# Performance work log

Measured on AMD Instinct MI355X. Metric: run time of the kernel, lower is better.

The kernel has to match this reference:

```python
import jax, jax.numpy as jnp
import numpy as np

N_NODES = 50000
N_EDGES = 800000
F_NODE = 128
F_EDGE = 64
Z_DIM = 2 * F_NODE + F_EDGE  # 320
BN_EPS = 1e-5


def _params(key):
    ks = jax.random.split(key, 16)
    s = 1.0 / np.sqrt(Z_DIM)
    p = {}
    for li, k4 in zip((1, 2), (ks[:8], ks[8:])):
        p[f"Wf{li}"] = jax.random.uniform(k4[0], (Z_DIM, F_NODE), jnp.float32, -s, s)
        p[f"bf{li}"] = jax.random.uniform(k4[1], (F_NODE,), jnp.float32, -s, s)
        p[f"Ws{li}"] = jax.random.uniform(k4[2], (Z_DIM, F_NODE), jnp.float32, -s, s)
        p[f"bs{li}"] = jax.random.uniform(k4[3], (F_NODE,), jnp.float32, -s, s)
        p[f"gamma{li}"] = jnp.ones((F_NODE,), jnp.float32)
        p[f"beta{li}"] = jnp.zeros((F_NODE,), jnp.float32)
        p[f"rmean{li}"] = jax.random.normal(k4[4], (F_NODE,), jnp.float32) * 0.1
        p[f"rvar{li}"] = jax.random.uniform(k4[5], (F_NODE,), jnp.float32, 0.5, 1.5)
    return p


def setup_inputs() -> dict:
    key = jax.random.key(0)
    k1, k2, k3, kp = jax.random.split(key, 4)
    inp = {
        "x": jax.random.normal(k1, (N_NODES, F_NODE), jnp.float32),
        "edge_index": jax.random.randint(k2, (2, N_EDGES), 0, N_NODES, jnp.int64),
        "edge_attr": jax.random.normal(k3, (N_EDGES, F_EDGE), jnp.float32),
    }
    inp.update(_params(kp))
    return inp


def _cgconv(x, src, dst, edge_attr, Wf, bf, Ws, bs, gamma, beta, rmean, rvar):
    # z = [x_i, x_j, edge_attr] with i = target (dst), j = source (src)
    z = jnp.concatenate([x[dst], x[src], edge_attr], axis=-1)  # [E, 320]
    msg = jax.nn.sigmoid(z @ Wf + bf) * jax.nn.softplus(z @ Ws + bs)  # [E, F]
    n = x.shape[0]
    summed = jax.ops.segment_sum(msg, dst, num_segments=n)  # [N, F]
    cnt = jax.ops.segment_sum(jnp.ones((dst.shape[0],), x.dtype), dst, num_segments=n)
    out = summed / jnp.maximum(cnt, 1.0)[:, None]  # mean aggregation
    out = (out - rmean) * jax.lax.rsqrt(rvar + BN_EPS) * gamma + beta  # BN (eval)
    return out + x  # residual


def reference(x, edge_index, edge_attr,
              Wf1, bf1, Ws1, bs1, gamma1, beta1, rmean1, rvar1,
              Wf2, bf2, Ws2, bs2, gamma2, beta2, rmean2, rvar2):
    src, dst = edge_index[0], edge_index[1]
    x = _cgconv(x, src, dst, edge_attr, Wf1, bf1, Ws1, bs1, gamma1, beta1, rmean1, rvar1)
    # dropout_p = 0.0 -> identity
    x = _cgconv(x, src, dst, edge_attr, Wf2, bf2, Ws2, bs2, gamma2, beta2, rmean2, rvar2)
    return x
```

## Files before the change

### kernel.cpp

```cpp
#include <hip/hip_runtime.h>
#include <math.h>

#define FN 128
#define FE 64
#define EPS 1e-5f

typedef __attribute__((ext_vector_type(8))) short bf16x8;
typedef __attribute__((ext_vector_type(4))) float f32x4;

__device__ __forceinline__ float bf2f(unsigned int u_low16) {
    union { unsigned int i; float f; } v; v.i = u_low16 << 16; return v.f;
}
__device__ __forceinline__ float bf2f_hi(unsigned int u) {
    union { unsigned int i; float f; } v; v.i = u & 0xffff0000u; return v.f;
}
__device__ __forceinline__ unsigned short f2bf(float f) {
    union { float f; unsigned int i; } v; v.f = f;
    unsigned int r = v.i + 0x7FFFu + ((v.i >> 16) & 1u);
    return (unsigned short)(r >> 16);
}
__device__ __forceinline__ unsigned int pack2bf(float a, float b) {
    return (unsigned int)f2bf(a) | ((unsigned int)f2bf(b) << 16);
}
__device__ __forceinline__ unsigned int pack4fp8(float a, float b, float c, float d) {
    int u = __builtin_amdgcn_cvt_pk_fp8_f32(a, b, 0, false);
    u = __builtin_amdgcn_cvt_pk_fp8_f32(c, d, u, true);
    return (unsigned int)u;
}
__device__ __forceinline__ float actfn(float f, float s) {
    float sig = __builtin_amdgcn_rcpf(1.0f + __expf(-f));
    float sp = fmaxf(s, 0.0f) + __logf(1.0f + __expf(-fabsf(s)));
    return sig * sp;
}

__global__ void hist_kernel(const int* __restrict__ edst, int* __restrict__ hist, int ne) {
    int e = blockIdx.x * 256 + threadIdx.x;
    if (e < ne) atomicAdd(&hist[edst[e]], 1);
}

__global__ __launch_bounds__(1024) void scan_kernel(
    const int* __restrict__ hist, int* __restrict__ cursor, int nn)
{
    __shared__ int buf[1024];
    int t = threadIdx.x;
    int per = (nn + 1023) >> 10;
    int lo = t * per, hi = min(lo + per, nn);
    int s = 0;
    for (int i = lo; i < hi; i++) s += hist[i];
    buf[t] = s;
    __syncthreads();
    int incl = s;
    for (int off = 1; off < 1024; off <<= 1) {
        int tmp = (t >= off) ? buf[t - off] : 0;
        __syncthreads();
        incl += tmp;
        buf[t] = incl;
        __syncthreads();
    }
    int run = incl - s;
    for (int i = lo; i < hi; i++) { cursor[i] = run; run += hist[i]; }
}

__global__ void scatter_kernel(const int* __restrict__ edst, int* __restrict__ cursor,
                               int* __restrict__ perm, int ne)
{
    int e = blockIdx.x * 256 + threadIdx.x;
    if (e < ne) {
        int pos = atomicAdd(&cursor[edst[e]], 1);
        perm[pos] = e;
    }
}

__global__ __launch_bounds__(256) void convert_ea_kernel(
    const float* __restrict__ EA, const int* __restrict__ perm,
    unsigned char* __restrict__ ea8, int ne)
{
    int pos = blockIdx.x * 256 + threadIdx.x;
    if (pos >= ne) return;
    const float* src = EA + (size_t)perm[pos] * FE;
    uint4 outv[4];
    unsigned int* o = (unsigned int*)outv;
#pragma unroll
    for (int q = 0; q < 16; q++) {
        float4 v = *(const float4*)(src + q * 4);
        o[q] = pack4fp8(v.x, v.y, v.z, v.w);
    }
    uint4* dst = (uint4*)(ea8 + (size_t)pos * 64);
#pragma unroll
    for (int q = 0; q < 4; q++) dst[q] = outv[q];
}

__global__ __launch_bounds__(256, 4) void node_gemm(
    const float* __restrict__ X, const float* __restrict__ Wf,
    const float* __restrict__ Ws, unsigned short* __restrict__ A, int nnodes)
{
    __shared__ unsigned short Xs[128][128];
    __shared__ unsigned short Wt[64][128];
    const int t = threadIdx.x;
    const int m0 = blockIdx.x * 128;
    const int c0 = blockIdx.y * 64;
    const int part = c0 >> 7;
    const float* Bsrc = ((part < 2) ? Wf : Ws) + (part & 1) * 128 * 128 + (c0 & 127);

    {
        int row = t & 127;
        int kh = t >> 7;
        int m = m0 + row;
        const float* src = X + (size_t)(m < nnodes ? m : 0) * FN + kh * 64;
        int swz = (row & 7) << 3;
#pragma unroll
        for (int q = 0; q < 8; q++) {
            float4 v0 = *(const float4*)(src + q * 8);
            float4 v1 = *(const float4*)(src + q * 8 + 4);
            unsigned int u0 = pack2bf(v0.x, v0.y), u1 = pack2bf(v0.z, v0.w);
            unsigned int u2 = pack2bf(v1.x, v1.y), u3 = pack2bf(v1.z, v1.w);
            int kk = (kh * 64 + q * 8) ^ swz;
            *(uint4*)&Xs[row][kk] = make_uint4(u0, u1, u2, u3);
        }
    }
    {
        int n = t & 63;
        int kq = t >> 6;
        int swz = (n & 7) << 3;
#pragma unroll
        for (int q = 0; q < 16; q++) {
            int k = kq * 32 + q * 2;
            unsigned int u = pack2bf(Bsrc[(size_t)k * FN + n], Bsrc[(size_t)(k + 1) * FN + n]);
            *(unsigned int*)&Wt[n][k ^ swz] = u;
        }
    }
    __syncthreads();

    const int wv = t >> 6, lane = t & 63;
    const int mw = (wv & 1) * 64;
    const int nw = (wv >> 1) * 32;
    f32x4 acc[4][2];
#pragma unroll
    for (int mt = 0; mt < 4; mt++)
#pragma unroll
        for (int nt = 0; nt < 2; nt++) acc[mt][nt] = (f32x4){0.f, 0.f, 0.f, 0.f};

#pragma unroll
    for (int ks = 0; ks < 4; ks++) {
        int kb = ks * 32 + ((lane >> 4) << 3);
        bf16x8 a[4], b[2];
#pragma unroll
        for (int mt = 0; mt < 4; mt++) {
            int row = mw + mt * 16 + (lane & 15);
            a[mt] = *(const bf16x8*)&Xs[row][kb ^ ((row & 7) << 3)];
        }
#pragma unroll
        for (int nt = 0; nt < 2; nt++) {
            int n = nw + nt * 16 + (lane & 15);
            b[nt] = *(const bf16x8*)&Wt[n][kb ^ ((n & 7) << 3)];
        }
#pragma unroll
        for (int mt = 0; mt < 4; mt++)
#pragma unroll
            for (int nt = 0; nt < 2; nt++)
                acc[mt][nt] = __builtin_amdgcn_mfma_f32_16x16x32_bf16(
                    a[mt], b[nt], acc[mt][nt], 0, 0, 0);
    }

#pragma unroll
    for (int mt = 0; mt < 4; mt++) {
        int m = m0 + mw + mt * 16 + ((lane >> 4) << 2);
#pragma unroll
        for (int nt = 0; nt < 2; nt++) {
            int n = c0 + nw + nt * 16 + (lane & 15);
#pragma unroll
            for (int r = 0; r < 4; r++)
                if (m + r < nnodes)
                    A[(size_t)(m + r) * 512 + n] = f2bf(acc[mt][nt][r]);
        }
    }
}

__global__ __launch_bounds__(256, 4) void edge_kernel(
    const unsigned short* __restrict__ A, const float* __restrict__ EA,
    const unsigned char* __restrict__ ea8,
    const int* __restrict__ esrc, const int* __restrict__ edst,
    const int* __restrict__ perm,
    const float* __restrict__ Wf, const float* __restrict__ Ws,
    const float* __restrict__ bfv, const float* __restrict__ bsv,
    float* __restrict__ summed, int nedges)
{
    __shared__ unsigned char Wlds[2][128][64];
    __shared__ unsigned short Ebuf[4][64][36];

    const int t = threadIdx.x;
    const int w = t >> 6, lane = t & 63;
    const int ebase = blockIdx.x * 256 + w * 64;

    {
        int col = t & 127;
        int half = t >> 7;
        int swz = (col & 7) << 3;
#pragma unroll 2
        for (int mat = 0; mat < 2; mat++) {
            const float* Wsrc = (mat == 0 ? Wf : Ws) + 256 * FN + col;
#pragma unroll
            for (int q = 0; q < 8; q++) {
                int k = half * 32 + q * 4;
                unsigned int u = pack4fp8(Wsrc[(size_t)k * FN],
                                          Wsrc[(size_t)(k + 1) * FN],
                                          Wsrc[(size_t)(k + 2) * FN],
                                          Wsrc[(size_t)(k + 3) * FN]);
                *(unsigned int*)&Wlds[mat][col][k ^ swz] = u;
            }
        }
    }

    int e = ebase + lane;
    bool valid = (e < nedges);
    int eC = valid ? e : (nedges - 1);
    const int pe = perm[eC];
    const int mydst = edst[pe];
    const int mysrc = esrc[pe];

    unsigned long long flushAfter;
    {
        int prevd = __shfl(mydst, (lane + 63) & 63);
        unsigned long long chg = __ballot(lane > 0 && (mydst != prevd));
        flushAfter = (chg >> 1) | (1ull << 63) | (1ull << 31);
    }

    int vmask[4];
    const unsigned short* dB[4];
    const unsigned short* sB[4];
#pragma unroll
    for (int nt = 0; nt < 4; nt++) {
        int el = nt * 16 + (lane & 15);
        vmask[nt] = (ebase + el < nedges) ? 1 : 0;
        int dn = __shfl(mydst, el);
        int sn = __shfl(mysrc, el);
        dB[nt] = A + (size_t)dn * 512;
        sB[nt] = A + (size_t)sn * 512 + 128;
    }

    long Eb[4][2];
    if (ea8) {
        const int koff8 = (lane >> 4) << 3;
#pragma unroll
        for (int nt = 0; nt < 4; nt++) {
            int row = ebase + nt * 16 + (lane & 15);
            if (row >= nedges) row = nedges - 1;
            const unsigned char* p = ea8 + (size_t)row * 64 + koff8;
            Eb[nt][0] = *(const long*)(const void*)(p);
            Eb[nt][1] = *(const long*)(const void*)(p + 32);
        }
    } else {
        const int koff = (lane >> 4) << 3;
#pragma unroll
        for (int nt = 0; nt < 4; nt++) {
            int el = nt * 16 + (lane & 15);
            int pr = __shfl(pe, el);
            const float* p = EA + (size_t)pr * FE + koff;
#pragma unroll
            for (int kk = 0; kk < 2; kk++) {
                float4 v0 = *(const float4*)(p + kk * 32);
                float4 v1 = *(const float4*)(p + kk * 32 + 4);
                unsigned int lo = pack4fp8(v0.x, v0.y, v0.z, v0.w);
                unsigned int hi = pack4fp8(v1.x, v1.y, v1.z, v1.w);
                Eb[nt][kk] = (long)(((unsigned long long)hi << 32) | lo);
            }
        }
    }
    __syncthreads();

    const int colo = (lane >> 4) << 2;
    const int cc = lane & 31;
    const int h = lane >> 5;

#pragma unroll 1
    for (int cb = 0; cb < 4; cb++) {
        const int c0 = cb * 32;

        uint2 gdf[4][2], gsf[4][2], gds[4][2], gss[4][2];
#pragma unroll
        for (int nt = 0; nt < 4; nt++)
#pragma unroll
            for (int mt = 0; mt < 2; mt++) {
                int off = c0 + mt * 16 + colo;
                gdf[nt][mt] = *(const uint2*)(const void*)(dB[nt] + off);
                gsf[nt][mt] = *(const uint2*)(const void*)(sB[nt] + off);
                gds[nt][mt] = *(const uint2*)(const void*)(dB[nt] + 256 + off);
                gss[nt][mt] = *(const uint2*)(const void*)(sB[nt] + 256 + off);
            }

        float4 bF[2], bS[2];
#pragma unroll
        for (int mt = 0; mt < 2; mt++) {
            bF[mt] = *(const float4*)(bfv + c0 + mt * 16 + colo);
            bS[mt] = *(const float4*)(bsv + c0 + mt * 16 + colo);
        }

        f32x4 accF[2][4], accS[2][4];
#pragma unroll
        for (int mt = 0; mt < 2; mt++)
#pragma unroll
            for (int nt = 0; nt < 4; nt++) {
                accF[mt][nt] = (f32x4){bF[mt].x, bF[mt].y, bF[mt].z, bF[mt].w};
                accS[mt][nt] = (f32x4){bS[mt].x, bS[mt].y, bS[mt].z, bS[mt].w};
            }
#pragma unroll
        for (int kk = 0; kk < 2; kk++) {
            long aF[2], aS[2];
#pragma unroll
            for (int mt = 0; mt < 2; mt++) {
                int col = c0 + mt * 16 + (lane & 15);
                int kidx = ((kk << 5) + ((lane >> 4) << 3)) ^ ((col & 7) << 3);
                aF[mt] = *(const long*)(const void*)&Wlds[0][col][kidx];
                aS[mt] = *(const long*)(const void*)&Wlds[1][col][kidx];
            }
#pragma unroll
            for (int mt = 0; mt < 2; mt++)
#pragma unroll
                for (int nt = 0; nt < 4; nt++) {
                    accF[mt][nt] = __builtin_amdgcn_mfma_f32_16x16x32_fp8_fp8(
                        aF[mt], Eb[nt][kk], accF[mt][nt], 0, 0, 0);
                    accS[mt][nt] = __builtin_amdgcn_mfma_f32_16x16x32_fp8_fp8(
                        aS[mt], Eb[nt][kk], accS[mt][nt], 0, 0, 0);
                }
        }

#pragma unroll
        for (int nt = 0; nt < 4; nt++) {
            int edge = nt * 16 + (lane & 15);
#pragma unroll
            for (int mt = 0; mt < 2; mt++) {
                f32x4 F = accF[mt][nt], S = accS[mt][nt];
                uint2 a0 = gdf[nt][mt], a1 = gsf[nt][mt];
                uint2 b0 = gds[nt][mt], b1 = gss[nt][mt];
                F[0] += bf2f(a0.x & 0xffffu) + bf2f(a1.x & 0xffffu);
                F[1] += bf2f_hi(a0.x)        + bf2f_hi(a1.x);
                F[2] += bf2f(a0.y & 0xffffu) + bf2f(a1.y & 0xffffu);
                F[3] += bf2f_hi(a0.y)        + bf2f_hi(a1.y);
                S[0] += bf2f(b0.x & 0xffffu) + bf2f(b1.x & 0xffffu);
                S[1] += bf2f_hi(b0.x)        + bf2f_hi(b1.x);
                S[2] += bf2f(b0.y & 0xffffu) + bf2f(b1.y & 0xffffu);
                S[3] += bf2f_hi(b0.y)        + bf2f_hi(b1.y);
                float m0 = actfn(F[0], S[0]);
                float m1 = actfn(F[1], S[1]);
                float m2 = actfn(F[2], S[2]);
                float m3 = actfn(F[3], S[3]);
                if (!vmask[nt]) { m0 = m1 = m2 = m3 = 0.0f; }
                uint2 mw = make_uint2(pack2bf(m0, m1), pack2bf(m2, m3));
                *(uint2*)&Ebuf[w][edge][mt * 16 + colo] = mw;
            }
        }

        asm volatile("" ::: "memory");

        {
            int ebit0 = h << 5;
            float run = 0.f;
#pragma unroll 1
            for (int q = 0; q < 32; q++) {
                int e2 = ebit0 + q;
                run += bf2f((unsigned int)Ebuf[w][e2][cc]);
                int d = __shfl(mydst, e2);
                if ((flushAfter >> e2) & 1ull) {
                    atomicAdd(&summed[(size_t)d * FN + c0 + cc], run);
                    run = 0.f;
                }
            }
        }

        asm volatile("" ::: "memory");
    }
}

__global__ __launch_bounds__(256) void finalize_kernel(
    const float* __restrict__ summed, const int* __restrict__ hist,
    const float* xin,
    const float* __restrict__ gamma, const float* __restrict__ beta,
    const float* __restrict__ rmean, const float* __restrict__ rvar,
    float* out, int nnodes)
{
    int idx = blockIdx.x * 256 + threadIdx.x;
    if (idx >= nnodes * FN) return;
    int n = idx >> 7, c = idx & (FN - 1);
    float cnt = (float)hist[n];
    float mean = summed[idx] / fmaxf(cnt, 1.0f);
    float y = (mean - rmean[c]) * rsqrtf(rvar[c] + EPS) * gamma[c] + beta[c] + xin[idx];
    out[idx] = y;
}

extern "C" void kernel_launch(void* const* d_in, const int* in_sizes, int n_in,
                              void* d_out, int out_size, void* d_ws, size_t ws_size,
                              hipStream_t stream)
{
    const float* x    = (const float*)d_in[0];
    const int*   eidx = (const int*)d_in[1];
    const float* ea   = (const float*)d_in[2];
    const float* Wf1 = (const float*)d_in[3],  * bf1 = (const float*)d_in[4];
    const float* Ws1 = (const float*)d_in[5],  * bs1 = (const float*)d_in[6];
    const float* g1  = (const float*)d_in[7],  * be1 = (const float*)d_in[8];
    const float* rm1 = (const float*)d_in[9],  * rv1 = (const float*)d_in[10];
    const float* Wf2 = (const float*)d_in[11], * bf2 = (const float*)d_in[12];
    const float* Ws2 = (const float*)d_in[13], * bs2 = (const float*)d_in[14];
    const float* g2  = (const float*)d_in[15], * be2 = (const float*)d_in[16];
    const float* rm2 = (const float*)d_in[17], * rv2 = (const float*)d_in[18];
    float* out = (float*)d_out;

    const int NN = in_sizes[0] / FN;
    const int NE = in_sizes[2] / FE;
    const int* esrc = eidx;
    const int* edst = eidx + NE;

    char* wsp = (char*)d_ws;
    unsigned short* A = (unsigned short*)wsp;            wsp += (size_t)NN * 512 * 2;
    float* summed     = (float*)wsp;                     wsp += (size_t)NN * FN * 4;
    int* hist         = (int*)wsp;                       wsp += (size_t)NN * 4;
    int* perm         = (int*)wsp;                       wsp += (size_t)NE * 4;
    size_t used       = (size_t)(wsp - (char*)d_ws);
    size_t needEA8    = used + (size_t)NE * 64;
    unsigned char* ea8 = (ws_size >= needEA8) ? (unsigned char*)wsp : nullptr;
    int* cursor       = (int*)summed;

    const int egrid = (NE + 255) / 256;
    const int ngrid = (NN + 127) / 128;
    const int fgrid = (NN * FN + 255) / 256;

    (void)hipMemsetAsync(hist, 0, (size_t)NN * 4, stream);
    hist_kernel<<<egrid, 256, 0, stream>>>(edst, hist, NE);
    scan_kernel<<<1, 1024, 0, stream>>>(hist, cursor, NN);
    scatter_kernel<<<egrid, 256, 0, stream>>>(edst, cursor, perm, NE);
    if (ea8) convert_ea_kernel<<<egrid, 256, 0, stream>>>(ea, perm, ea8, NE);

    (void)hipMemsetAsync(summed, 0, (size_t)NN * FN * 4, stream);
    node_gemm<<<dim3(ngrid, 8), 256, 0, stream>>>(x, Wf1, Ws1, A, NN);
    edge_kernel<<<egrid, 256, 0, stream>>>(A, ea, ea8, esrc, edst, perm, Wf1, Ws1, bf1, bs1, summed, NE);
    finalize_kernel<<<fgrid, 256, 0, stream>>>(summed, hist, x, g1, be1, rm1, rv1, out, NN);

    (void)hipMemsetAsync(summed, 0, (size_t)NN * FN * 4, stream);
    node_gemm<<<dim3(ngrid, 8), 256, 0, stream>>>(out, Wf2, Ws2, A, NN);
    edge_kernel<<<egrid, 256, 0, stream>>>(A, ea, ea8, esrc, edst, perm, Wf2, Ws2, bf2, bs2, summed, NE);
    finalize_kernel<<<fgrid, 256, 0, stream>>>(summed, hist, out, g2, be2, rm2, rv2, out, NN);
}
```

Baseline: 768.2 us.

## Store source-node projections in fp8 and convert edge attrs via inverse permutation

```diff
diff --git a/kernel.cpp b/kernel.cpp
--- a/kernel.cpp
+++ b/kernel.cpp
@@ -26,6 +26,9 @@
     int u = __builtin_amdgcn_cvt_pk_fp8_f32(a, b, 0, false);
     u = __builtin_amdgcn_cvt_pk_fp8_f32(c, d, u, true);
     return (unsigned int)u;
+}
+__device__ __forceinline__ unsigned char f2fp8(float v) {
+    return (unsigned char)(__builtin_amdgcn_cvt_pk_fp8_f32(v, v, 0, false) & 0xff);
 }
 __device__ __forceinline__ float actfn(float f, float s) {
     float sig = __builtin_amdgcn_rcpf(1.0f + __expf(-f));
@@ -62,22 +65,23 @@
 }
 
 __global__ void scatter_kernel(const int* __restrict__ edst, int* __restrict__ cursor,
-                               int* __restrict__ perm, int ne)
+                               int* __restrict__ perm, int* __restrict__ invp, int ne)
 {
     int e = blockIdx.x * 256 + threadIdx.x;
     if (e < ne) {
         int pos = atomicAdd(&cursor[edst[e]], 1);
         perm[pos] = e;
+        invp[e] = pos;
     }
 }
 
 __global__ __launch_bounds__(256) void convert_ea_kernel(
-    const float* __restrict__ EA, const int* __restrict__ perm,
+    const float* __restrict__ EA, const int* __restrict__ invp,
     unsigned char* __restrict__ ea8, int ne)
 {
-    int pos = blockIdx.x * 256 + threadIdx.x;
-    if (pos >= ne) return;
-    const float* src = EA + (size_t)perm[pos] * FE;
+    int e = blockIdx.x * 256 + threadIdx.x;
+    if (e >= ne) return;
+    const float* src = EA + (size_t)e * FE;
     uint4 outv[4];
     unsigned int* o = (unsigned int*)outv;
 #pragma unroll
@@ -85,14 +89,15 @@
         float4 v = *(const float4*)(src + q * 4);
         o[q] = pack4fp8(v.x, v.y, v.z, v.w);
     }
-    uint4* dst = (uint4*)(ea8 + (size_t)pos * 64);
+    uint4* dst = (uint4*)(ea8 + (size_t)invp[e] * 64);
 #pragma unroll
     for (int q = 0; q < 4; q++) dst[q] = outv[q];
 }
 
 __global__ __launch_bounds__(256, 4) void node_gemm(
     const float* __restrict__ X, const float* __restrict__ Wf,
-    const float* __restrict__ Ws, unsigned short* __restrict__ A, int nnodes)
+    const float* __restrict__ Ws, unsigned short* __restrict__ Ad,
+    unsigned char* __restrict__ As8, int nnodes)
 {
     __shared__ unsigned short Xs[128][128];
     __shared__ unsigned short Wt[64][128];
@@ -162,23 +167,29 @@
                     a[mt], b[nt], acc[mt][nt], 0, 0, 0);
     }
 
+    const int colbase = ((part >> 1) << 7) + (c0 & 127) + nw;
 #pragma unroll
     for (int mt = 0; mt < 4; mt++) {
         int m = m0 + mw + mt * 16 + ((lane >> 4) << 2);
 #pragma unroll
         for (int nt = 0; nt < 2; nt++) {
-            int n = c0 + nw + nt * 16 + (lane & 15);
-#pragma unroll
-            for (int r = 0; r < 4; r++)
-                if (m + r < nnodes)
-                    A[(size_t)(m + r) * 512 + n] = f2bf(acc[mt][nt][r]);
+            int col = colbase + nt * 16 + (lane & 15);
+#pragma unroll
+            for (int r = 0; r < 4; r++) {
+                if (m + r < nnodes) {
+                    if (part & 1)
+                        As8[(size_t)(m + r) * 256 + col] = f2fp8(acc[mt][nt][r]);
+                    else
+                        Ad[(size_t)(m + r) * 256 + col] = f2bf(acc[mt][nt][r]);
+                }
+            }
         }
     }
 }
 
 __global__ __launch_bounds__(256, 4) void edge_kernel(
-    const unsigned short* __restrict__ A, const float* __restrict__ EA,
-    const unsigned char* __restrict__ ea8,
+    const unsigned short* __restrict__ Ad, const unsigned char* __restrict__ As8,
+    const float* __restrict__ EA, const unsigned char* __restrict__ ea8,
     const int* __restrict__ esrc, const int* __restrict__ edst,
     const int* __restrict__ perm,
     const float* __restrict__ Wf, const float* __restrict__ Ws,
@@ -227,19 +238,19 @@
 
     int vmask[4];
     const unsigned short* dB[4];
-    const unsigned short* sB[4];
+    const unsigned char* sB[4];
 #pragma unroll
     for (int nt = 0; nt < 4; nt++) {
         int el = nt * 16 + (lane & 15);
         vmask[nt] = (ebase + el < nedges) ? 1 : 0;
         int dn = __shfl(mydst, el);
         int sn = __shfl(mysrc, el);
-        dB[nt] = A + (size_t)dn * 512;
-        sB[nt] = A + (size_t)sn * 512 + 128;
+        dB[nt] = Ad + (size_t)dn * 256;
+        sB[nt] = As8 + (size_t)sn * 256;
     }
 
     long Eb[4][2];
-    if (ea8) {
+    {
         const int koff8 = (lane >> 4) << 3;
 #pragma unroll
         for (int nt = 0; nt < 4; nt++) {
@@ -249,22 +260,6 @@
             Eb[nt][0] = *(const long*)(const void*)(p);
             Eb[nt][1] = *(const long*)(const void*)(p + 32);
         }
-    } else {
-        const int koff = (lane >> 4) << 3;
-#pragma unroll
-        for (int nt = 0; nt < 4; nt++) {
-            int el = nt * 16 + (lane & 15);
-            int pr = __shfl(pe, el);
-            const float* p = EA + (size_t)pr * FE + koff;
-#pragma unroll
-            for (int kk = 0; kk < 2; kk++) {
-                float4 v0 = *(const float4*)(p + kk * 32);
-                float4 v1 = *(const float4*)(p + kk * 32 + 4);
-                unsigned int lo = pack4fp8(v0.x, v0.y, v0.z, v0.w);
-                unsigned int hi = pack4fp8(v1.x, v1.y, v1.z, v1.w);
-                Eb[nt][kk] = (long)(((unsigned long long)hi << 32) | lo);
-            }
-        }
     }
     __syncthreads();
 
@@ -276,16 +271,17 @@
     for (int cb = 0; cb < 4; cb++) {
         const int c0 = cb * 32;
 
-        uint2 gdf[4][2], gsf[4][2], gds[4][2], gss[4][2];
+        uint2 gdf[4][2], gds[4][2];
+        unsigned int gsf8[4][2], gss8[4][2];
 #pragma unroll
         for (int nt = 0; nt < 4; nt++)
 #pragma unroll
             for (int mt = 0; mt < 2; mt++) {
                 int off = c0 + mt * 16 + colo;
                 gdf[nt][mt] = *(const uint2*)(const void*)(dB[nt] + off);
-                gsf[nt][mt] = *(const uint2*)(const void*)(sB[nt] + off);
-                gds[nt][mt] = *(const uint2*)(const void*)(dB[nt] + 256 + off);
-                gss[nt][mt] = *(const uint2*)(const void*)(sB[nt] + 256 + off);
+                gds[nt][mt] = *(const uint2*)(const void*)(dB[nt] + 128 + off);
+                gsf8[nt][mt] = *(const unsigned int*)(const void*)(sB[nt] + off);
+                gss8[nt][mt] = *(const unsigned int*)(const void*)(sB[nt] + 128 + off);
             }
 
         float4 bF[2], bS[2];
@@ -330,16 +326,16 @@
 #pragma unroll
             for (int mt = 0; mt < 2; mt++) {
                 f32x4 F = accF[mt][nt], S = accS[mt][nt];
-                uint2 a0 = gdf[nt][mt], a1 = gsf[nt][mt];
-                uint2 b0 = gds[nt][mt], b1 = gss[nt][mt];
-                F[0] += bf2f(a0.x & 0xffffu) + bf2f(a1.x & 0xffffu);
-                F[1] += bf2f_hi(a0.x)        + bf2f_hi(a1.x);
-                F[2] += bf2f(a0.y & 0xffffu) + bf2f(a1.y & 0xffffu);
-                F[3] += bf2f_hi(a0.y)        + bf2f_hi(a1.y);
-                S[0] += bf2f(b0.x & 0xffffu) + bf2f(b1.x & 0xffffu);
-                S[1] += bf2f_hi(b0.x)        + bf2f_hi(b1.x);
-                S[2] += bf2f(b0.y & 0xffffu) + bf2f(b1.y & 0xffffu);
-                S[3] += bf2f_hi(b0.y)        + bf2f_hi(b1.y);
+                uint2 a0 = gdf[nt][mt], b0 = gds[nt][mt];
+                unsigned int a1 = gsf8[nt][mt], b1 = gss8[nt][mt];
+                F[0] += bf2f(a0.x & 0xffffu) + __builtin_amdgcn_cvt_f32_fp8(a1, 0);
+                F[1] += bf2f_hi(a0.x)        + __builtin_amdgcn_cvt_f32_fp8(a1, 1);
+                F[2] += bf2f(a0.y & 0xffffu) + __builtin_amdgcn_cvt_f32_fp8(a1, 2);
+                F[3] += bf2f_hi(a0.y)        + __builtin_amdgcn_cvt_f32_fp8(a1, 3);
+                S[0] += bf2f(b0.x & 0xffffu) + __builtin_amdgcn_cvt_f32_fp8(b1, 0);
+                S[1] += bf2f_hi(b0.x)        + __builtin_amdgcn_cvt_f32_fp8(b1, 1);
+                S[2] += bf2f(b0.y & 0xffffu) + __builtin_amdgcn_cvt_f32_fp8(b1, 2);
+                S[3] += bf2f_hi(b0.y)        + __builtin_amdgcn_cvt_f32_fp8(b1, 3);
                 float m0 = actfn(F[0], S[0]);
                 float m1 = actfn(F[1], S[1]);
                 float m2 = actfn(F[2], S[2]);
@@ -410,13 +406,13 @@
     const int* edst = eidx + NE;
 
     char* wsp = (char*)d_ws;
-    unsigned short* A = (unsigned short*)wsp;            wsp += (size_t)NN * 512 * 2;
+    unsigned short* Ad  = (unsigned short*)wsp;          wsp += (size_t)NN * 256 * 2;
+    unsigned char*  As8 = (unsigned char*)wsp;           wsp += (size_t)NN * 256;
     float* summed     = (float*)wsp;                     wsp += (size_t)NN * FN * 4;
     int* hist         = (int*)wsp;                       wsp += (size_t)NN * 4;
     int* perm         = (int*)wsp;                       wsp += (size_t)NE * 4;
-    size_t used       = (size_t)(wsp - (char*)d_ws);
-    size_t needEA8    = used + (size_t)NE * 64;
-    unsigned char* ea8 = (ws_size >= needEA8) ? (unsigned char*)wsp : nullptr;
+    int* invp         = (int*)wsp;                       wsp += (size_t)NE * 4;
+    unsigned char* ea8 = (unsigned char*)wsp;            wsp += (size_t)NE * 64;
     int* cursor       = (int*)summed;
 
     const int egrid = (NE + 255) / 256;
@@ -426,16 +422,16 @@
     (void)hipMemsetAsync(hist, 0, (size_t)NN * 4, stream);
     hist_kernel<<<egrid, 256, 0, stream>>>(edst, hist, NE);
     scan_kernel<<<1, 1024, 0, stream>>>(hist, cursor, NN);
-    scatter_kernel<<<egrid, 256, 0, stream>>>(edst, cursor, perm, NE);
-    if (ea8) convert_ea_kernel<<<egrid, 256, 0, stream>>>(ea, perm, ea8, NE);
+    scatter_kernel<<<egrid, 256, 0, stream>>>(edst, cursor, perm, invp, NE);
+    convert_ea_kernel<<<egrid, 256, 0, stream>>>(ea, invp, ea8, NE);
 
     (void)hipMemsetAsync(summed, 0, (size_t)NN * FN * 4, stream);
-    node_gemm<<<dim3(ngrid, 8), 256, 0, stream>>>(x, Wf1, Ws1, A, NN);
-    edge_kernel<<<egrid, 256, 0, stream>>>(A, ea, ea8, esrc, edst, perm, Wf1, Ws1, bf1, bs1, summed, NE);
+    node_gemm<<<dim3(ngrid, 8), 256, 0, stream>>>(x, Wf1, Ws1, Ad, As8, NN);
+    edge_kernel<<<egrid, 256, 0, stream>>>(Ad, As8, ea, ea8, esrc, edst, perm, Wf1, Ws1, bf1, bs1, summed, NE);
     finalize_kernel<<<fgrid, 256, 0, stream>>>(summed, hist, x, g1, be1, rm1, rv1, out, NN);
 
     (void)hipMemsetAsync(summed, 0, (size_t)NN * FN * 4, stream);
-    node_gemm<<<dim3(ngrid, 8), 256, 0, stream>>>(out, Wf2, Ws2, A, NN);
-    edge_kernel<<<egrid, 256, 0, stream>>>(A, ea, ea8, esrc, edst, perm, Wf2, Ws2, bf2, bs2, summed, NE);
+    node_gemm<<<dim3(ngrid, 8), 256, 0, stream>>>(out, Wf2, Ws2, Ad, As8, NN);
+    edge_kernel<<<egrid, 256, 0, stream>>>(Ad, As8, ea, ea8, esrc, edst, perm, Wf2, Ws2, bf2, bs2, summed, NE);
     finalize_kernel<<<fgrid, 256, 0, stream>>>(summed, hist, out, g2, be2, rm2, rv2, out, NN);
 }
```

Result: slower. 825.3 us (+7.4%).
